# Kernel tuning notes

Hardware: AMD Instinct MI355X
Metric: run time of the kernel (lower is better)

## Reference

```python
import jax, jax.numpy as jnp
import numpy as np

ALPHA = 0.2          # LeakyReLU negative slope
MASK_VAL = -9e15     # matches torch -9000000000000000.0


def setup_inputs() -> dict:
    key = jax.random.key(0)
    k1, k2, k3, k4 = jax.random.split(key, 4)
    B, N, F_IN, F_OUT, DEG = 64, 1024, 64, 64, 8
    atoms = jax.random.normal(k1, (B, N, F_IN), dtype=jnp.float32)
    edges = jax.random.randint(k2, (B, N, DEG), 0, N, dtype=jnp.int64)
    # xavier_uniform with gain=1.414
    def xavier(k, shape, gain=1.414):
        fan_in, fan_out = shape[0], shape[1]
        bound = gain * np.sqrt(6.0 / (fan_in + fan_out))
        return jax.random.uniform(k, shape, jnp.float32, -bound, bound)
    W = xavier(k3, (F_IN, F_OUT))
    a = xavier(k4, (2 * F_OUT, 1))
    return {"atoms": atoms, "edges": edges, "W": W, "a": a}


def reference(atoms, edges, W, a):
    B, N, _ = atoms.shape
    F_OUT = W.shape[1]
    # h = atom @ W per graph -> [B, N, F_OUT]
    h = jnp.einsum('bnf,fo->bno', atoms, W)
    # Decompose concat-attention: e_ij = leakyrelu(h_i . a1 + h_j . a2)
    a1 = a[:F_OUT, 0]
    a2 = a[F_OUT:, 0]
    s1 = h @ a1  # [B, N]
    s2 = h @ a2  # [B, N]
    e = s1[:, :, None] + s2[:, None, :]  # [B, N, N]
    e = jnp.where(e > 0, e, ALPHA * e)   # LeakyReLU
    # Build adjacency mask from edge lists: adj[b, i, edges[b,i,d]] = True
    b_idx = jnp.arange(B)[:, None, None]
    i_idx = jnp.arange(N)[None, :, None]
    adj = jnp.zeros((B, N, N), dtype=bool).at[b_idx, i_idx, edges].set(True)
    e = jnp.where(adj, e, MASK_VAL)
    attn = jax.nn.softmax(e, axis=-1)    # [B, N, N]
    h_prime = jnp.einsum('bij,bjo->bio', attn, h)
    return jax.nn.elu(h_prime)
```

## Files before the change

### kernel.cpp

```cpp
#include <hip/hip_runtime.h>
#include <math.h>

#define BATCH 64
#define NNODE 1024
#define FDIM 64
#define DEG 8
#define ALPHA 0.2f

typedef __attribute__((ext_vector_type(8))) short bf16x8;
typedef __attribute__((ext_vector_type(4))) float f32x4;

__device__ __forceinline__ short f2bf(float f) {
    union { float f; unsigned u; } v; v.f = f;
    unsigned r = v.u + 0x7fffu + ((v.u >> 16) & 1u);
    return (short)(r >> 16);
}

__global__ void gat_k0(const float* __restrict__ W, const float* __restrict__ a,
                       float* __restrict__ wa) {
    const int k = threadIdx.x;
    float p1 = 0.f, p2 = 0.f;
    #pragma unroll
    for (int j = 0; j < FDIM; ++j) {
        const float w = W[k * FDIM + j];
        p1 = fmaf(w, a[j], p1);
        p2 = fmaf(w, a[FDIM + j], p2);
    }
    wa[k] = p1; wa[FDIM + k] = p2;
}

__global__ __launch_bounds__(256) void gat_k1(
    const float* __restrict__ atoms,
    const float* __restrict__ W,
    const float* __restrict__ wa,
    float* __restrict__ h,
    float* __restrict__ s1,
    float* __restrict__ s2)
{
    const int lane = threadIdx.x & 63;
    const int wv   = threadIdx.x >> 6;
    const int l16  = lane & 15;
    const int qd   = lane >> 4;
    const int rowbase = (blockIdx.x * 4 + wv) * 16;

    bf16x8 Bw[2][4];
    #pragma unroll
    for (int ks = 0; ks < 2; ++ks)
        #pragma unroll
        for (int t = 0; t < 4; ++t)
            #pragma unroll
            for (int j = 0; j < 8; ++j)
                Bw[ks][t][j] = f2bf(W[(ks * 32 + qd * 8 + j) * FDIM + t * 16 + l16]);

    bf16x8 Bs[2];
    #pragma unroll
    for (int ks = 0; ks < 2; ++ks)
        #pragma unroll
        for (int j = 0; j < 8; ++j) {
            const int k = ks * 32 + qd * 8 + j;
            const float v = (l16 == 0) ? wa[k] : ((l16 == 1) ? wa[FDIM + k] : 0.f);
            Bs[ks][j] = f2bf(v);
        }

    const float* __restrict__ ar = atoms + (size_t)(rowbase + l16) * FDIM;
    bf16x8 A[2];
    #pragma unroll
    for (int ks = 0; ks < 2; ++ks) {
        const float4 p0 = *(const float4*)(ar + ks * 32 + qd * 8);
        const float4 p1 = *(const float4*)(ar + ks * 32 + qd * 8 + 4);
        A[ks][0] = f2bf(p0.x); A[ks][1] = f2bf(p0.y);
        A[ks][2] = f2bf(p0.z); A[ks][3] = f2bf(p0.w);
        A[ks][4] = f2bf(p1.x); A[ks][5] = f2bf(p1.y);
        A[ks][6] = f2bf(p1.z); A[ks][7] = f2bf(p1.w);
    }

    f32x4 C[4] = {{0,0,0,0},{0,0,0,0},{0,0,0,0},{0,0,0,0}};
    f32x4 Cs = {0,0,0,0};
    #pragma unroll
    for (int ks = 0; ks < 2; ++ks) {
        #pragma unroll
        for (int t = 0; t < 4; ++t)
            C[t] = __builtin_amdgcn_mfma_f32_16x16x32_bf16(A[ks], Bw[ks][t], C[t], 0, 0, 0);
        Cs = __builtin_amdgcn_mfma_f32_16x16x32_bf16(A[ks], Bs[ks], Cs, 0, 0, 0);
    }

    #pragma unroll
    for (int t = 0; t < 4; ++t)
        #pragma unroll
        for (int r = 0; r < 4; ++r)
            h[(size_t)(rowbase + qd * 4 + r) * FDIM + t * 16 + l16] = C[t][r];

    if (l16 < 2) {
        float* sp = (l16 == 0) ? s1 : s2;
        #pragma unroll
        for (int r = 0; r < 4; ++r)
            sp[rowbase + qd * 4 + r] = Cs[r];
    }
}

__global__ __launch_bounds__(256) void gat_k2(
    const float* __restrict__ h,
    const float* __restrict__ s1g,
    const float* __restrict__ s2g,
    const int*   __restrict__ edges,
    float* __restrict__ out)
{
    __shared__ float s2l[NNODE];
    __shared__ int   el[64 * DEG];
    __shared__ float s1l[64];

    const int bid   = blockIdx.x;
    const int slot  = bid >> 3;
    const int b     = (bid & 7) + 8 * (slot & 7);
    const int chunk = slot >> 3;
    const int rowbase = b * NNODE + chunk * 64;

    const int tid = threadIdx.x;
    ((float4*)s2l)[tid] = ((const float4*)(s2g + b * NNODE))[tid];
    ((int2*)el)[tid]    = ((const int2*)(edges + (size_t)rowbase * DEG))[tid];
    if (tid < 64) s1l[tid] = s1g[rowbase + tid];
    __syncthreads();

    const int lane = tid & 63;
    const int wv   = tid >> 6;
    const float* __restrict__ hb = h + (size_t)b * NNODE * FDIM;

    #pragma unroll 2
    for (int i = 0; i < 16; ++i) {
        const int rl = wv * 16 + i;
        int ej[DEG];
        #pragma unroll
        for (int k = 0; k < DEG; ++k) ej[k] = el[rl * DEG + k];

        const float si = s1l[rl];
        float e[DEG], mx = -INFINITY;
        #pragma unroll
        for (int k = 0; k < DEG; ++k) {
            float v = si + s2l[ej[k]];
            v = (v > 0.f) ? v : ALPHA * v;
            e[k] = v; mx = fmaxf(mx, v);
        }
        float wgt[DEG], wsum = 0.f;
        #pragma unroll
        for (int k = 0; k < DEG; ++k) {
            bool kp = true;
            #pragma unroll
            for (int m = 0; m < DEG; ++m)
                if (m < k && ej[m] == ej[k]) kp = false;
            const float w = kp ? __expf(e[k] - mx) : 0.f;
            wgt[k] = w; wsum += w;
        }
        const float inv = 1.f / wsum;

        float acc = 0.f;
        #pragma unroll
        for (int k = 0; k < DEG; ++k)
            acc = fmaf(wgt[k] * inv, hb[(size_t)ej[k] * FDIM + lane], acc);

        out[(size_t)(rowbase + rl) * FDIM + lane] = (acc > 0.f) ? acc : (__expf(acc) - 1.f);
    }
}

extern "C" void kernel_launch(void* const* d_in, const int* in_sizes, int n_in,
                              void* d_out, int out_size, void* d_ws, size_t ws_size,
                              hipStream_t stream) {
    const float* atoms = (const float*)d_in[0];
    const int*   edges = (const int*)d_in[1];
    const float* W     = (const float*)d_in[2];
    const float* a     = (const float*)d_in[3];
    float* out = (float*)d_out;

    const int rows = BATCH * NNODE;

    float* h  = (float*)d_ws;
    float* s1 = h + (size_t)rows * FDIM;
    float* s2 = s1 + rows;
    float* wa = s2 + rows;

    gat_k0<<<1, 64, 0, stream>>>(W, a, wa);
    gat_k1<<<rows / 64, 256, 0, stream>>>(atoms, W, wa, h, s1, s2);
    gat_k2<<<rows / 64, 256, 0, stream>>>(h, s1, s2, edges, out);
}
```

Before: 101.4 us.

## Fuse projection, scoring and neighbor aggregation into one kernel with h in LDS

Replaces three kernels with a single fused kernel. Each block recomputes the full per-graph h (stored as swizzled bf16 in shared memory) and s1/s2, then handles a quarter of the rows. The softmax weights are computed cooperatively across 4 lanes per row, and the aggregation reads h from LDS instead of global memory. This removes the global round trip for h and the launch overhead, at the cost of recomputing the projection four times per graph, adding bf16 rounding on h, and using large LDS that allows only one block per CU.

```diff
diff --git a/kernel.cpp b/kernel.cpp
--- a/kernel.cpp
+++ b/kernel.cpp
@@ -1,11 +1,13 @@
 #include <hip/hip_runtime.h>
 #include <math.h>
 
-#define BATCH 64
-#define NNODE 1024
-#define FDIM 64
-#define DEG 8
-#define ALPHA 0.2f
+#define BATCH  64
+#define NNODE  1024
+#define FDIM   64
+#define DEG    8
+#define ALPHA  0.2f
+#define COPIES 4
+#define RPB    (NNODE / COPIES)
 
 typedef __attribute__((ext_vector_type(8))) short bf16x8;
 typedef __attribute__((ext_vector_type(4))) float f32x4;
@@ -15,149 +17,186 @@
     unsigned r = v.u + 0x7fffu + ((v.u >> 16) & 1u);
     return (short)(r >> 16);
 }
-
-__global__ void gat_k0(const float* __restrict__ W, const float* __restrict__ a,
-                       float* __restrict__ wa) {
-    const int k = threadIdx.x;
-    float p1 = 0.f, p2 = 0.f;
-    #pragma unroll
-    for (int j = 0; j < FDIM; ++j) {
-        const float w = W[k * FDIM + j];
-        p1 = fmaf(w, a[j], p1);
-        p2 = fmaf(w, a[FDIM + j], p2);
-    }
-    wa[k] = p1; wa[FDIM + k] = p2;
-}
-
-__global__ __launch_bounds__(256) void gat_k1(
+__device__ __forceinline__ float bflo(unsigned d) {
+    union { unsigned u; float f; } v; v.u = d << 16; return v.f;
+}
+__device__ __forceinline__ float bfhi(unsigned d) {
+    union { unsigned u; float f; } v; v.u = d & 0xffff0000u; return v.f;
+}
+
+__global__ __launch_bounds__(1024) void gat_fused(
     const float* __restrict__ atoms,
+    const int*   __restrict__ edges,
     const float* __restrict__ W,
-    const float* __restrict__ wa,
-    float* __restrict__ h,
-    float* __restrict__ s1,
-    float* __restrict__ s2)
+    const float* __restrict__ a,
+    float* __restrict__ out)
 {
-    const int lane = threadIdx.x & 63;
-    const int wv   = threadIdx.x >> 6;
+    __shared__ unsigned long long hsh[NNODE * FDIM / 4];
+    __shared__ float  s1l[NNODE];
+    __shared__ float  s2l[NNODE];
+    __shared__ float2 wal2[FDIM];
+    __shared__ unsigned awl[RPB * DEG * 2];
+
+    const int bid = blockIdx.x;
+    const int c = (bid >> 3) & 3;
+    const int b = (bid & 7) | ((bid >> 5) << 3);
+
+    const int tid  = threadIdx.x;
+    const int lane = tid & 63;
+    const int wv   = tid >> 6;
     const int l16  = lane & 15;
     const int qd   = lane >> 4;
-    const int rowbase = (blockIdx.x * 4 + wv) * 16;
-
-    bf16x8 Bw[2][4];
+
+    if (wv == 0) {
+        float p1 = 0.f, p2 = 0.f;
+        #pragma unroll
+        for (int j = 0; j < FDIM; ++j) {
+            const float w = W[lane * FDIM + j];
+            p1 = fmaf(w, a[j], p1);
+            p2 = fmaf(w, a[FDIM + j], p2);
+        }
+        wal2[lane] = make_float2(p1, p2);
+    }
+
+    bf16x8 Aw[2][4];
     #pragma unroll
     for (int ks = 0; ks < 2; ++ks)
         #pragma unroll
         for (int t = 0; t < 4; ++t)
             #pragma unroll
             for (int j = 0; j < 8; ++j)
-                Bw[ks][t][j] = f2bf(W[(ks * 32 + qd * 8 + j) * FDIM + t * 16 + l16]);
-
-    bf16x8 Bs[2];
+                Aw[ks][t][j] = f2bf(W[(ks * 32 + qd * 8 + j) * FDIM + t * 16 + l16]);
+
+    __syncthreads();
+
+    float2 wv12[2][8];
     #pragma unroll
     for (int ks = 0; ks < 2; ++ks)
         #pragma unroll
-        for (int j = 0; j < 8; ++j) {
-            const int k = ks * 32 + qd * 8 + j;
-            const float v = (l16 == 0) ? wa[k] : ((l16 == 1) ? wa[FDIM + k] : 0.f);
-            Bs[ks][j] = f2bf(v);
-        }
-
-    const float* __restrict__ ar = atoms + (size_t)(rowbase + l16) * FDIM;
-    bf16x8 A[2];
+        for (int j = 0; j < 8; ++j)
+            wv12[ks][j] = wal2[ks * 32 + qd * 8 + j];
+
+    const float* __restrict__ ab = atoms + (size_t)b * NNODE * FDIM;
     #pragma unroll
-    for (int ks = 0; ks < 2; ++ks) {
-        const float4 p0 = *(const float4*)(ar + ks * 32 + qd * 8);
-        const float4 p1 = *(const float4*)(ar + ks * 32 + qd * 8 + 4);
-        A[ks][0] = f2bf(p0.x); A[ks][1] = f2bf(p0.y);
-        A[ks][2] = f2bf(p0.z); A[ks][3] = f2bf(p0.w);
-        A[ks][4] = f2bf(p1.x); A[ks][5] = f2bf(p1.y);
-        A[ks][6] = f2bf(p1.z); A[ks][7] = f2bf(p1.w);
-    }
-
-    f32x4 C[4] = {{0,0,0,0},{0,0,0,0},{0,0,0,0},{0,0,0,0}};
-    f32x4 Cs = {0,0,0,0};
-    #pragma unroll
-    for (int ks = 0; ks < 2; ++ks) {
-        #pragma unroll
-        for (int t = 0; t < 4; ++t)
-            C[t] = __builtin_amdgcn_mfma_f32_16x16x32_bf16(A[ks], Bw[ks][t], C[t], 0, 0, 0);
-        Cs = __builtin_amdgcn_mfma_f32_16x16x32_bf16(A[ks], Bs[ks], Cs, 0, 0, 0);
-    }
-
-    #pragma unroll
-    for (int t = 0; t < 4; ++t)
-        #pragma unroll
-        for (int r = 0; r < 4; ++r)
-            h[(size_t)(rowbase + qd * 4 + r) * FDIM + t * 16 + l16] = C[t][r];
-
-    if (l16 < 2) {
-        float* sp = (l16 == 0) ? s1 : s2;
-        #pragma unroll
-        for (int r = 0; r < 4; ++r)
-            sp[rowbase + qd * 4 + r] = Cs[r];
-    }
-}
-
-__global__ __launch_bounds__(256) void gat_k2(
-    const float* __restrict__ h,
-    const float* __restrict__ s1g,
-    const float* __restrict__ s2g,
-    const int*   __restrict__ edges,
-    float* __restrict__ out)
-{
-    __shared__ float s2l[NNODE];
-    __shared__ int   el[64 * DEG];
-    __shared__ float s1l[64];
-
-    const int bid   = blockIdx.x;
-    const int slot  = bid >> 3;
-    const int b     = (bid & 7) + 8 * (slot & 7);
-    const int chunk = slot >> 3;
-    const int rowbase = b * NNODE + chunk * 64;
-
-    const int tid = threadIdx.x;
-    ((float4*)s2l)[tid] = ((const float4*)(s2g + b * NNODE))[tid];
-    ((int2*)el)[tid]    = ((const int2*)(edges + (size_t)rowbase * DEG))[tid];
-    if (tid < 64) s1l[tid] = s1g[rowbase + tid];
+    for (int tt = 0; tt < 4; ++tt) {
+        const int node = wv * 64 + tt * 16 + l16;
+        const float* __restrict__ ar = ab + (size_t)node * FDIM;
+
+        bf16x8 Bv[2];
+        float sp1 = 0.f, sp2 = 0.f;
+        #pragma unroll
+        for (int ks = 0; ks < 2; ++ks) {
+            const float4 p0 = *(const float4*)(ar + ks * 32 + qd * 8);
+            const float4 p1 = *(const float4*)(ar + ks * 32 + qd * 8 + 4);
+            Bv[ks][0] = f2bf(p0.x); Bv[ks][1] = f2bf(p0.y);
+            Bv[ks][2] = f2bf(p0.z); Bv[ks][3] = f2bf(p0.w);
+            Bv[ks][4] = f2bf(p1.x); Bv[ks][5] = f2bf(p1.y);
+            Bv[ks][6] = f2bf(p1.z); Bv[ks][7] = f2bf(p1.w);
+            sp1 = fmaf(p0.x, wv12[ks][0].x, sp1); sp2 = fmaf(p0.x, wv12[ks][0].y, sp2);
+            sp1 = fmaf(p0.y, wv12[ks][1].x, sp1); sp2 = fmaf(p0.y, wv12[ks][1].y, sp2);
+            sp1 = fmaf(p0.z, wv12[ks][2].x, sp1); sp2 = fmaf(p0.z, wv12[ks][2].y, sp2);
+            sp1 = fmaf(p0.w, wv12[ks][3].x, sp1); sp2 = fmaf(p0.w, wv12[ks][3].y, sp2);
+            sp1 = fmaf(p1.x, wv12[ks][4].x, sp1); sp2 = fmaf(p1.x, wv12[ks][4].y, sp2);
+            sp1 = fmaf(p1.y, wv12[ks][5].x, sp1); sp2 = fmaf(p1.y, wv12[ks][5].y, sp2);
+            sp1 = fmaf(p1.z, wv12[ks][6].x, sp1); sp2 = fmaf(p1.z, wv12[ks][6].y, sp2);
+            sp1 = fmaf(p1.w, wv12[ks][7].x, sp1); sp2 = fmaf(p1.w, wv12[ks][7].y, sp2);
+        }
+        sp1 += __shfl_xor(sp1, 16); sp1 += __shfl_xor(sp1, 32);
+        sp2 += __shfl_xor(sp2, 16); sp2 += __shfl_xor(sp2, 32);
+        if (qd == 0) { s1l[node] = sp1; s2l[node] = sp2; }
+
+        f32x4 C[4] = {{0,0,0,0},{0,0,0,0},{0,0,0,0},{0,0,0,0}};
+        #pragma unroll
+        for (int ks = 0; ks < 2; ++ks)
+            #pragma unroll
+            for (int t = 0; t < 4; ++t)
+                C[t] = __builtin_amdgcn_mfma_f32_16x16x32_bf16(Aw[ks][t], Bv[ks], C[t], 0, 0, 0);
+
+        #pragma unroll
+        for (int t = 0; t < 4; ++t) {
+            union { unsigned short s[4]; unsigned long long v; } pk;
+            pk.s[0] = (unsigned short)f2bf(C[t][0]);
+            pk.s[1] = (unsigned short)f2bf(C[t][1]);
+            pk.s[2] = (unsigned short)f2bf(C[t][2]);
+            pk.s[3] = (unsigned short)f2bf(C[t][3]);
+            const unsigned byte = (unsigned)node * 128u +
+                (((unsigned)(t * 32 + qd * 8)) ^ ((unsigned)(node & 15) << 3));
+            *(unsigned long long*)((char*)hsh + byte) = pk.v;
+        }
+    }
     __syncthreads();
 
-    const int lane = tid & 63;
-    const int wv   = tid >> 6;
-    const float* __restrict__ hb = h + (size_t)b * NNODE * FDIM;
-
+    {
+        const int r = tid >> 2;
+        const int j = tid & 3;
+        const int grow = b * NNODE + c * RPB + r;
+        const int2 ed = *(const int2*)(edges + (size_t)grow * DEG + 2 * j);
+
+        const int ax = __shfl_xor(ed.x, 1), ay = __shfl_xor(ed.y, 1);
+        const int bx = __shfl_xor(ed.x, 2), by = __shfl_xor(ed.y, 2);
+        const int cx = __shfl_xor(ax, 2),   cy = __shfl_xor(ay, 2);
+
+        int e8[8];
+        #pragma unroll
+        for (int o = 0; o < 4; ++o) {
+            const int d = o ^ j;
+            e8[2*o]   = (d == 0) ? ed.x : (d == 1) ? ax : (d == 2) ? bx : cx;
+            e8[2*o+1] = (d == 0) ? ed.y : (d == 1) ? ay : (d == 2) ? by : cy;
+        }
+
+        const float s1v = s1l[c * RPB + r];
+        float lA = s1v + s2l[ed.x];
+        float lB = s1v + s2l[ed.y];
+        lA = (lA > 0.f) ? lA : ALPHA * lA;
+        lB = (lB > 0.f) ? lB : ALPHA * lB;
+
+        float m = fmaxf(lA, lB);
+        m = fmaxf(m, __shfl_xor(m, 1));
+        m = fmaxf(m, __shfl_xor(m, 2));
+
+        bool dupA = false, dupB = false;
+        #pragma unroll
+        for (int mm = 0; mm < 8; ++mm) {
+            dupA = dupA || ((mm < 2 * j)     && (e8[mm] == ed.x));
+            dupB = dupB || ((mm < 2 * j + 1) && (e8[mm] == ed.y));
+        }
+
+        float wA = dupA ? 0.f : __expf(lA - m);
+        float wB = dupB ? 0.f : __expf(lB - m);
+        float s = wA + wB;
+        s += __shfl_xor(s, 1);
+        s += __shfl_xor(s, 2);
+        const float inv = 1.f / s;
+        wA *= inv; wB *= inv;
+
+        union { float f; unsigned u; } fa, fb; fa.f = wA; fb.f = wB;
+        uint4 st;
+        st.x = (unsigned)(ed.x * 128 + ((ed.x & 15) << 3)); st.y = fa.u;
+        st.z = (unsigned)(ed.y * 128 + ((ed.y & 15) << 3)); st.w = fb.u;
+        *(uint4*)(awl + (r * DEG + 2 * j) * 2) = st;
+    }
+    __syncthreads();
+
+    const int l32 = lane & 31;
+    const int h32 = lane >> 5;
+    float* __restrict__ ob = out + (size_t)(b * NNODE + c * RPB) * FDIM;
     #pragma unroll 2
-    for (int i = 0; i < 16; ++i) {
-        const int rl = wv * 16 + i;
-        int ej[DEG];
-        #pragma unroll
-        for (int k = 0; k < DEG; ++k) ej[k] = el[rl * DEG + k];
-
-        const float si = s1l[rl];
-        float e[DEG], mx = -INFINITY;
+    for (int p = 0; p < 8; ++p) {
+        const int rowl = wv * 16 + 2 * p + h32;
+        const uint2* __restrict__ awp = (const uint2*)(awl + rowl * DEG * 2);
+        float a0 = 0.f, a1 = 0.f;
         #pragma unroll
         for (int k = 0; k < DEG; ++k) {
-            float v = si + s2l[ej[k]];
-            v = (v > 0.f) ? v : ALPHA * v;
-            e[k] = v; mx = fmaxf(mx, v);
-        }
-        float wgt[DEG], wsum = 0.f;
-        #pragma unroll
-        for (int k = 0; k < DEG; ++k) {
-            bool kp = true;
-            #pragma unroll
-            for (int m = 0; m < DEG; ++m)
-                if (m < k && ej[m] == ej[k]) kp = false;
-            const float w = kp ? __expf(e[k] - mx) : 0.f;
-            wgt[k] = w; wsum += w;
-        }
-        const float inv = 1.f / wsum;
-
-        float acc = 0.f;
-        #pragma unroll
-        for (int k = 0; k < DEG; ++k)
-            acc = fmaf(wgt[k] * inv, hb[(size_t)ej[k] * FDIM + lane], acc);
-
-        out[(size_t)(rowbase + rl) * FDIM + lane] = (acc > 0.f) ? acc : (__expf(acc) - 1.f);
+            const uint2 t = awp[k];
+            const unsigned d = *(const unsigned*)((const char*)hsh +
+                                   (t.x ^ (unsigned)(l32 << 2)));
+            union { unsigned u; float f; } wu; wu.u = t.y;
+            a0 = fmaf(wu.f, bflo(d), a0);
+            a1 = fmaf(wu.f, bfhi(d), a1);
+        }
+        a0 = (a0 > 0.f) ? a0 : (__expf(a0) - 1.f);
+        a1 = (a1 > 0.f) ? a1 : (__expf(a1) - 1.f);
+        *(float2*)(ob + (size_t)rowl * FDIM + 2 * l32) = make_float2(a0, a1);
     }
 }
 
@@ -170,14 +209,5 @@
     const float* a     = (const float*)d_in[3];
     float* out = (float*)d_out;
 
-    const int rows = BATCH * NNODE;
-
-    float* h  = (float*)d_ws;
-    float* s1 = h + (size_t)rows * FDIM;
-    float* s2 = s1 + rows;
-    float* wa = s2 + rows;
-
-    gat_k0<<<1, 64, 0, stream>>>(W, a, wa);
-    gat_k1<<<rows / 64, 256, 0, stream>>>(atoms, W, wa, h, s1, s2);
-    gat_k2<<<rows / 64, 256, 0, stream>>>(h, s1, s2, edges, out);
-}
+    gat_fused<<<BATCH * COPIES, 1024, 0, stream>>>(atoms, edges, W, a, out);
+}
```

Result: faster. 86.83 us (-14.4%).
